# Performance work log

Measured on AMD Instinct MI355X. Metric: run time of the kernel, lower is better.

Reference implementation:

```python
import jax, jax.numpy as jnp
import numpy as np

ITERATIONS = 4

def setup_inputs() -> dict:
    key = jax.random.key(0)
    x = jax.random.normal(key, (16, 8192, 256), dtype=jnp.float32)
    return {"x": x}

def reference(x):
    # x: [B, S, D]; whiten features (last dim) using stats over axis=1 (sequence)
    B, S, D = x.shape
    m = jnp.mean(x, axis=1, keepdims=True)          # [B, 1, D]
    xn = x - m                                      # centered
    # covariance: [B, D, D]
    sigma = jnp.einsum('bsd,bse->bde', xn, xn) / (S - 1)
    # Newton-Schulz iteration for inverse matrix square root
    tr = jnp.trace(sigma, axis1=1, axis2=2)[:, None, None]   # [B,1,1]
    sigma_n = sigma / tr
    eye = jnp.eye(D, dtype=x.dtype)
    P = jnp.broadcast_to(eye, (B, D, D))
    for _ in range(ITERATIONS):
        P = 1.5 * P - 0.5 * (P @ P @ P @ sigma_n)
    wm = P / jnp.sqrt(tr)                           # whitening matrix [B, D, D]
    decorrelated = jnp.einsum('bsd,bde->bse', xn, wm)
    return decorrelated
```

## Files before the change

kernel.cpp:

```cpp
#include <hip/hip_runtime.h>

#define BB 16
#define SS 8192
#define DD 256

typedef __attribute__((ext_vector_type(8))) short bf16x8;
typedef __attribute__((ext_vector_type(4))) short bf16x4;
typedef __attribute__((ext_vector_type(4))) float f32x4;

__device__ __forceinline__ unsigned short f2bf(float f) {
    union { float f; unsigned u; } v; v.f = f;
    unsigned r = v.u + 0x7FFFu + ((v.u >> 16) & 1u);
    return (unsigned short)(r >> 16);
}
__device__ __forceinline__ float bf2f(unsigned short u) {
    union { unsigned u; float f; } cv; cv.u = (unsigned)u << 16; return cv.f;
}
__device__ __forceinline__ unsigned pack2(float a, float b) {
    return (unsigned)f2bf(a) | ((unsigned)f2bf(b) << 16);
}
__device__ __forceinline__ void split_bf(float w, unsigned short& hi, unsigned short& lo) {
    hi = f2bf(w);
    lo = f2bf(w - bf2f(hi));
}

#define LTS 40

__global__ __launch_bounds__(512) void moment_kernel(const float* __restrict__ x,
                                                     float* __restrict__ partial,
                                                     float* __restrict__ sumx8) {
    const int kc = blockIdx.x;
    const int nh = blockIdx.y;
    const int b  = blockIdx.z;
    const float* xb = x + ((size_t)b * SS + (size_t)kc * 1024) * DD;

    __shared__ unsigned short Lt0[256 * LTS];
    __shared__ unsigned short Lt1[256 * LTS];
    __shared__ float csh[8 * 256];

    const int tid  = threadIdx.x;
    const int wave = tid >> 6;
    const int lane = tid & 63;
    const int lc   = lane & 15;
    const int lq   = lane >> 4;

    const int mrow0 = (wave & 3) * 64;
    const int ncol0 = nh * 128 + (wave >> 2) * 64;

    const int sg = tid >> 6;
    const int dg = tid & 63;
    const float* xt = xb + (size_t)(sg * 4) * DD + dg;

    f32x4 acc[4][4];
#pragma unroll
    for (int mi = 0; mi < 4; ++mi)
#pragma unroll
        for (int ni = 0; ni < 4; ++ni) acc[mi][ni] = (f32x4){0.f, 0.f, 0.f, 0.f};
    float cs[4] = {0.f, 0.f, 0.f, 0.f};

    float va[16], vb[16];

    auto LOAD = [&](float* v, int t) {
#pragma unroll
        for (int i = 0; i < 4; ++i)
#pragma unroll
            for (int j = 0; j < 4; ++j)
                v[i * 4 + j] = xt[(size_t)(t * 32 + i) * DD + 64 * j];
    };
    auto STAGE = [&](const float* v, unsigned short* Lw) {
        if (nh == 0) {
#pragma unroll
            for (int j = 0; j < 4; ++j)
                cs[j] += v[j] + v[4 + j] + v[8 + j] + v[12 + j];
        }
#pragma unroll
        for (int j = 0; j < 4; ++j) {
            uint2 w;
            w.x = pack2(v[j], v[4 + j]);
            w.y = pack2(v[8 + j], v[12 + j]);
            *(uint2*)&Lw[(dg + 64 * j) * LTS + sg * 4] = w;
        }
    };
    auto COMPUTE = [&](const unsigned short* Lr) {
        bf16x8 af[4], bfr[4];
#pragma unroll
        for (int mi = 0; mi < 4; ++mi)
            af[mi] = *(const bf16x8*)&Lr[(mrow0 + mi * 16 + lc) * LTS + lq * 8];
#pragma unroll
        for (int ni = 0; ni < 4; ++ni)
            bfr[ni] = *(const bf16x8*)&Lr[(ncol0 + ni * 16 + lc) * LTS + lq * 8];
#pragma unroll
        for (int mi = 0; mi < 4; ++mi)
#pragma unroll
            for (int ni = 0; ni < 4; ++ni)
                acc[mi][ni] = __builtin_amdgcn_mfma_f32_16x16x32_bf16(
                    af[mi], bfr[ni], acc[mi][ni], 0, 0, 0);
    };

    LOAD(va, 0);
    STAGE(va, Lt0);
    LOAD(vb, 1);
    __syncthreads();

    for (int tt = 0; tt < 16; ++tt) {
        const int t0 = 2 * tt;
        STAGE(vb, Lt1);
        if (t0 < 30) LOAD(va, t0 + 2);
        COMPUTE(Lt0);
        __syncthreads();
        if (t0 + 1 < 31) STAGE(va, Lt0);
        if (t0 + 1 < 30) LOAD(vb, t0 + 3);
        COMPUTE(Lt1);
        __syncthreads();
    }

    float* pp = partial + (size_t)(kc * 16 + b) * DD * DD;
#pragma unroll
    for (int mi = 0; mi < 4; ++mi)
#pragma unroll
        for (int ni = 0; ni < 4; ++ni) {
            const int row = mrow0 + mi * 16 + lq * 4;
            const int col = ncol0 + ni * 16 + lc;
#pragma unroll
            for (int r = 0; r < 4; ++r)
                pp[(size_t)(row + r) * DD + col] = acc[mi][ni][r];
        }

    if (nh == 0) {
        __syncthreads();
#pragma unroll
        for (int j = 0; j < 4; ++j) csh[sg * 256 + dg + 64 * j] = cs[j];
        __syncthreads();
        if (tid < 256) {
            float t0 = 0.f;
#pragma unroll
            for (int g = 0; g < 8; ++g) t0 += csh[g * 256 + tid];
            sumx8[(size_t)(kc * 16 + b) * DD + tid] = t0;
        }
    }
}

__global__ __launch_bounds__(256) void stats_kernel(const float* __restrict__ partial,
                                                    const float* __restrict__ sumx8,
                                                    float* __restrict__ m,
                                                    float* __restrict__ trbuf) {
    const int b = blockIdx.x;
    const int d = threadIdx.x;
    float sx = 0.f;
#pragma unroll
    for (int kc = 0; kc < 8; ++kc)
        sx += sumx8[(size_t)(kc * 16 + b) * DD + d];
    const float mean = sx * (1.0f / (float)SS);
    m[b * DD + d] = mean;
    float ds = 0.f;
#pragma unroll
    for (int kc = 0; kc < 8; ++kc)
        ds += partial[((size_t)(kc * 16 + b) * DD + d) * DD + d];
    const float diag = (ds - (float)SS * mean * mean) * (1.0f / (float)(SS - 1));
    __shared__ float red[256];
    red[d] = diag;
    __syncthreads();
    for (int off = 128; off > 0; off >>= 1) {
        if (d < off) red[d] += red[d + off];
        __syncthreads();
    }
    if (d == 0) {
        const float tr = red[0];
        trbuf[b]      = tr;
        trbuf[16 + b] = rsqrtf(tr);
        trbuf[32 + b] = 1.0f / tr;
    }
}

__global__ __launch_bounds__(256) void sigman_kernel(const float* __restrict__ partial,
                                                     const float* __restrict__ m,
                                                     const float* __restrict__ trbuf,
                                                     float* __restrict__ Xa) {
    const int b = blockIdx.y;
    const int d = blockIdx.x;
    const int e = threadIdx.x;
    const float itr = trbuf[32 + b];
    const float md = m[b * DD + d];
    const float me = m[b * DD + e];
    float s = 0.f;
#pragma unroll
    for (int kc = 0; kc < 8; ++kc)
        s += partial[((size_t)(kc * 16 + b) * DD + d) * DD + e];
    Xa[(size_t)b * DD * DD + (size_t)d * DD + e] =
        (s - (float)SS * md * me) * (1.0f / (float)(SS - 1)) * itr;
}

#define BTS 72
__global__ __launch_bounds__(256) void bmm_mfma(
    const float* __restrict__ A0, const float* __restrict__ B0, float* __restrict__ C0,
    int ta0, int tb0,
    const float* __restrict__ A1, const float* __restrict__ B1, float* __restrict__ C1,
    int ta1, int tb1) {
    const int by  = blockIdx.y;
    const int set = by >> 4;
    const int bb  = by & 15;
    const float* Ag = (set ? A1 : A0) + (size_t)bb * DD * DD;
    const float* Bg = (set ? B1 : B0) + (size_t)bb * DD * DD;
    float*       Cg = (set ? C1 : C0) + (size_t)bb * DD * DD;
    const int TA = set ? ta1 : ta0;
    const int TB = set ? tb1 : tb0;

    const int m0 = (blockIdx.x >> 2) * 64;
    const int n0 = (blockIdx.x & 3) * 64;

    __shared__ unsigned short Ahi[2][64 * BTS];
    __shared__ unsigned short Alo[2][64 * BTS];
    __shared__ unsigned short Bhi[2][64 * BTS];
    __shared__ unsigned short Blo[2][64 * BTS];

    const int tid  = threadIdx.x;
    const int wave = tid >> 6;
    const int lane = tid & 63;
    const int lc = lane & 15, lq = lane >> 4;
    const int mrow0 = (wave & 1) * 32;
    const int ncol0 = (wave >> 1) * 32;

    const int r  = tid >> 2;
    const int kl = (tid & 3) * 4;
    const float* Arow = Ag + (size_t)(m0 + r) * DD + kl;
    const float* Brow = Bg + (size_t)(n0 + r) * DD + kl;

    f32x4 acc[2][2];
#pragma unroll
    for (int mi = 0; mi < 2; ++mi)
#pragma unroll
        for (int ni = 0; ni < 2; ++ni) acc[mi][ni] = (f32x4){0.f, 0.f, 0.f, 0.f};

    float4 va0[4], vb0[4], va1[4], vb1[4];

    auto LOADC = [&](float4* va, float4* vb, int c) {
#pragma unroll
        for (int i = 0; i < 4; ++i) va[i] = *(const float4*)(Arow + c * 64 + i * 16);
#pragma unroll
        for (int i = 0; i < 4; ++i) vb[i] = *(const float4*)(Brow + c * 64 + i * 16);
    };
    auto STAGE_SIDE = [&](const float4* v, unsigned short* Shi, unsigned short* Slo,
                          int c, int gmn, int tflag) {
#pragma unroll
        for (int i = 0; i < 4; ++i) {
            float xv[4] = {v[i].x, v[i].y, v[i].z, v[i].w};
            unsigned short h[4], l[4];
#pragma unroll
            for (int j = 0; j < 4; ++j) {
                float wv = xv[j];
                if (tflag) {
                    const int gk = c * 64 + kl + i * 16 + j;
                    wv = ((gk == gmn) ? 1.5f : 0.0f) - 0.5f * wv;
                }
                split_bf(wv, h[j], l[j]);
            }
            unsigned short* ph = &Shi[r * BTS + kl + i * 16];
            *(unsigned*)&ph[0] = (unsigned)h[0] | ((unsigned)h[1] << 16);
            *(unsigned*)&ph[2] = (unsigned)h[2] | ((unsigned)h[3] << 16);
            unsigned short* pl = &Slo[r * BTS + kl + i * 16];
            *(unsigned*)&pl[0] = (unsigned)l[0] | ((unsigned)l[1] << 16);
            *(unsigned*)&pl[2] = (unsigned)l[2] | ((unsigned)l[3] << 16);
        }
    };
    auto STAGE = [&](const float4* va, const float4* vb, int c, int buf) {
        STAGE_SIDE(va, Ahi[buf], Alo[buf], c, m0 + r, TA);
        STAGE_SIDE(vb, Bhi[buf], Blo[buf], c, n0 + r, TB);
    };
    auto COMPUTE = [&](int buf) {
#pragma unroll
        for (int ks = 0; ks < 2; ++ks) {
            bf16x8 ah[2], al[2], bh[2], bl[2];
#pragma unroll
            for (int mi = 0; mi < 2; ++mi) {
                const int off = (mrow0 + mi * 16 + lc) * BTS + ks * 32 + lq * 8;
                ah[mi] = *(const bf16x8*)&Ahi[buf][off];
                al[mi] = *(const bf16x8*)&Alo[buf][off];
            }
#pragma unroll
            for (int ni = 0; ni < 2; ++ni) {
                const int off = (ncol0 + ni * 16 + lc) * BTS + ks * 32 + lq * 8;
                bh[ni] = *(const bf16x8*)&Bhi[buf][off];
                bl[ni] = *(const bf16x8*)&Blo[buf][off];
            }
#pragma unroll
            for (int mi = 0; mi < 2; ++mi)
#pragma unroll
                for (int ni = 0; ni < 2; ++ni) {
                    acc[mi][ni] = __builtin_amdgcn_mfma_f32_16x16x32_bf16(
                        al[mi], bh[ni], acc[mi][ni], 0, 0, 0);
                    acc[mi][ni] = __builtin_amdgcn_mfma_f32_16x16x32_bf16(
                        ah[mi], bl[ni], acc[mi][ni], 0, 0, 0);
                    acc[mi][ni] = __builtin_amdgcn_mfma_f32_16x16x32_bf16(
                        ah[mi], bh[ni], acc[mi][ni], 0, 0, 0);
                }
        }
    };

    LOADC(va0, vb0, 0);
    LOADC(va1, vb1, 1);
    STAGE(va0, vb0, 0, 0);
    __syncthreads();
#pragma unroll
    for (int cc = 0; cc < 2; ++cc) {
        const int c0 = 2 * cc;
        STAGE(va1, vb1, c0 + 1, 1);
        if (c0 + 2 < 4) LOADC(va0, vb0, c0 + 2);
        COMPUTE(0);
        __syncthreads();
        if (c0 + 2 < 4) STAGE(va0, vb0, c0 + 2, 0);
        if (c0 + 3 < 4) LOADC(va1, vb1, c0 + 3);
        COMPUTE(1);
        __syncthreads();
    }

#pragma unroll
    for (int mi = 0; mi < 2; ++mi)
#pragma unroll
        for (int ni = 0; ni < 2; ++ni) {
            const int row = m0 + mrow0 + mi * 16 + lq * 4;
            const int col = n0 + ncol0 + ni * 16 + lc;
#pragma unroll
            for (int rr = 0; rr < 4; ++rr)
                Cg[(size_t)(row + rr) * DD + col] = acc[mi][ni][rr];
        }
}

#define BSS 264
__global__ __launch_bounds__(256) void apply_kernel(const float* __restrict__ x,
                                                    const float* __restrict__ P,
                                                    const float* __restrict__ m,
                                                    const float* __restrict__ trbuf,
                                                    float* __restrict__ out) {
    const int st = blockIdx.x;
    const int nh = blockIdx.y;
    const int b  = blockIdx.z;
    const int s0 = st * 128;
    const int n0 = nh * 128;
    const float rs = trbuf[16 + b];
    const float* xb = x + (size_t)b * SS * DD;
    const float* Pb = P + (size_t)b * DD * DD;
    const float* mb = m + b * DD;
    float* ob = out + (size_t)b * SS * DD;

    __shared__ unsigned short Bs[128 * BSS];
    __shared__ unsigned short As[128 * LTS];
    __shared__ float corr[128];

    const int tid  = threadIdx.x;
    const int wave = tid >> 6;
    const int lane = tid & 63;
    const int lc = lane & 15, lq = lane >> 4;
    const int mrow0 = (wave & 1) * 64;
    const int ncol0 = (wave >> 1) * 64;

    {
        const int r = tid >> 1, h = tid & 1;
        const float* prow = Pb + (size_t)(n0 + r) * DD + h * 128;
        unsigned short* brow = &Bs[r * BSS + h * 128];
#pragma unroll
        for (int i = 0; i < 32; ++i) {
            float4 pv = *(const float4*)(prow + i * 4);
            *(unsigned*)&brow[i * 4]     = pack2(pv.x * rs, pv.y * rs);
            *(unsigned*)&brow[i * 4 + 2] = pack2(pv.z * rs, pv.w * rs);
        }
    }
    __syncthreads();

    if (tid < 128) {
        float s = 0.f;
        for (int k = 0; k < 256; ++k)
            s += mb[k] * bf2f(Bs[tid * BSS + k]);
        corr[tid] = s;
    }

    f32x4 acc[4][4];
#pragma unroll
    for (int mi = 0; mi < 4; ++mi)
#pragma unroll
        for (int ni = 0; ni < 4; ++ni) acc[mi][ni] = (f32x4){0.f, 0.f, 0.f, 0.f};

    const int r8 = tid >> 3;
    const int d4 = (tid & 7) * 4;
    const float* xt = xb + (size_t)(s0 + r8) * DD + d4;

    float4 va[4], vb[4];

    auto LOAD = [&](float4* v, int t) {
#pragma unroll
        for (int i = 0; i < 4; ++i)
            v[i] = *(const float4*)(xt + (size_t)t * 32 + (size_t)i * 32 * DD);
    };
    auto STAGE = [&](const float4* v) {
#pragma unroll
        for (int i = 0; i < 4; ++i) {
            uint2 w;
            w.x = pack2(v[i].x, v[i].y);
            w.y = pack2(v[i].z, v[i].w);
            *(uint2*)&As[(r8 + i * 32) * LTS + d4] = w;
        }
    };
    auto COMPUTE = [&](int t) {
        const int k0 = t * 32;
        bf16x8 af[4], bfr[4];
#pragma unroll
        for (int mi = 0; mi < 4; ++mi)
            af[mi] = *(const bf16x8*)&As[(mrow0 + mi * 16 + lc) * LTS + lq * 8];
#pragma unroll
        for (int ni = 0; ni < 4; ++ni)
            bfr[ni] = *(const bf16x8*)&Bs[(ncol0 + ni * 16 + lc) * BSS + k0 + lq * 8];
#pragma unroll
        for (int mi = 0; mi < 4; ++mi)
#pragma unroll
            for (int ni = 0; ni < 4; ++ni)
                acc[mi][ni] = __builtin_amdgcn_mfma_f32_16x16x32_bf16(
                    af[mi], bfr[ni], acc[mi][ni], 0, 0, 0);
    };

    LOAD(va, 0);
#pragma unroll
    for (int tt = 0; tt < 4; ++tt) {
        const int t0 = 2 * tt;
        __syncthreads();
        STAGE(va);
        if (t0 + 1 < 8) LOAD(vb, t0 + 1);
        __syncthreads();
        COMPUTE(t0);
        __syncthreads();
        STAGE(vb);
        if (t0 + 2 < 8) LOAD(va, t0 + 2);
        __syncthreads();
        COMPUTE(t0 + 1);
    }

#pragma unroll
    for (int mi = 0; mi < 4; ++mi)
#pragma unroll
        for (int ni = 0; ni < 4; ++ni) {
            const int row = s0 + mrow0 + mi * 16 + lq * 4;
            const int col = n0 + ncol0 + ni * 16 + lc;
            const float cv = corr[ncol0 + ni * 16 + lc];
#pragma unroll
            for (int r = 0; r < 4; ++r)
                ob[(size_t)(row + r) * DD + col] = acc[mi][ni][r] - cv;
        }
}

extern "C" void kernel_launch(void* const* d_in, const int* in_sizes, int n_in,
                              void* d_out, int out_size, void* d_ws, size_t ws_size,
                              hipStream_t stream) {
    const float* x = (const float*)d_in[0];
    float* out = (float*)d_out;
    float* ws = (float*)d_ws;

    const size_t MAT = (size_t)BB * DD * DD;
    float* partial = ws;
    float* sumx8 = partial + 8 * MAT;
    float* m     = sumx8 + 8 * BB * DD;
    float* trbuf = m + BB * DD;
    float* Xa    = trbuf + 64;
    float* Xb    = Xa + MAT;
    float* T     = Xb + MAT;
    float* Pa    = T + MAT;
    float* Pb    = Pa + MAT;

    moment_kernel<<<dim3(8, 2, 16), 512, 0, stream>>>(x, partial, sumx8);
    stats_kernel<<<16, 256, 0, stream>>>(partial, sumx8, m, trbuf);
    sigman_kernel<<<dim3(256, 16), 256, 0, stream>>>(partial, m, trbuf, Xa);

    bmm_mfma<<<dim3(16, 16), 256, 0, stream>>>(Xa, Xa, T, 1, 1,
                                               Xa, Xa, T, 1, 1);
    bmm_mfma<<<dim3(16, 16), 256, 0, stream>>>(Xa, T, Xb, 0, 0,
                                               Xa, T, Xb, 0, 0);
    bmm_mfma<<<dim3(16, 32), 256, 0, stream>>>(Xa, Xb, Pa, 1, 1,
                                               Xb, Xb, T, 1, 1);
    bmm_mfma<<<dim3(16, 16), 256, 0, stream>>>(Xb, T, Xa, 0, 0,
                                               Xb, T, Xa, 0, 0);
    bmm_mfma<<<dim3(16, 32), 256, 0, stream>>>(Pa, Xa, Pb, 0, 1,
                                               Xa, Xa, T, 1, 1);
    bmm_mfma<<<dim3(16, 16), 256, 0, stream>>>(Xa, T, Xb, 0, 0,
                                               Xa, T, Xb, 0, 0);
    bmm_mfma<<<dim3(16, 16), 256, 0, stream>>>(Pb, Xb, Pa, 0, 1,
                                               Pb, Xb, Pa, 0, 1);

    apply_kernel<<<dim3(64, 2, 16), 256, 0, stream>>>(x, Pa, m, trbuf, out);
}
```

Measured before the change: 379.1 us.

## Fuse stats into sigman kernel and load apply A-fragments directly from global

Merges the trace/mean stats kernel and the normalized-covariance kernel into one finalize kernel, where each block recomputes the mean and trace redundantly and then writes 16 rows of sigma_n. This removes one launch and the serial dependency between them. The apply kernel now loads x straight into MFMA A-fragment registers in bf16 and drops the LDS staging and the four barriers per iteration pair. The mean-correction dot product is also split across all 256 threads. The risks are less coalesced global reads of x in the apply kernel and redundant trace reductions in every finalize block.

After: 412.9 us. 1.09x slower.

```diff
diff --git a/kernel.cpp b/kernel.cpp
--- a/kernel.cpp
+++ b/kernel.cpp
@@ -1,4 +1,5 @@
 #include <hip/hip_runtime.h>
+#include <hip/hip_bf16.h>
 
 #define BB 16
 #define SS 8192
@@ -140,54 +141,57 @@
     }
 }
 
-__global__ __launch_bounds__(256) void stats_kernel(const float* __restrict__ partial,
-                                                    const float* __restrict__ sumx8,
-                                                    float* __restrict__ m,
-                                                    float* __restrict__ trbuf) {
-    const int b = blockIdx.x;
-    const int d = threadIdx.x;
+__global__ __launch_bounds__(256) void finalize_kernel(const float* __restrict__ partial,
+                                                       const float* __restrict__ sumx8,
+                                                       float* __restrict__ m,
+                                                       float* __restrict__ trbuf,
+                                                       float* __restrict__ Xa) {
+    const int g = blockIdx.x;
+    const int b = blockIdx.y;
+    const int t = threadIdx.x;
+
+    __shared__ float mean[256];
+    __shared__ float red[256];
+
     float sx = 0.f;
 #pragma unroll
     for (int kc = 0; kc < 8; ++kc)
-        sx += sumx8[(size_t)(kc * 16 + b) * DD + d];
-    const float mean = sx * (1.0f / (float)SS);
-    m[b * DD + d] = mean;
+        sx += sumx8[(size_t)(kc * 16 + b) * DD + t];
+    const float mu = sx * (1.0f / (float)SS);
+    mean[t] = mu;
+    if (g == 0) m[b * DD + t] = mu;
+
     float ds = 0.f;
 #pragma unroll
     for (int kc = 0; kc < 8; ++kc)
-        ds += partial[((size_t)(kc * 16 + b) * DD + d) * DD + d];
-    const float diag = (ds - (float)SS * mean * mean) * (1.0f / (float)(SS - 1));
-    __shared__ float red[256];
-    red[d] = diag;
+        ds += partial[((size_t)(kc * 16 + b) * DD + t) * DD + t];
+    red[t] = (ds - (float)SS * mu * mu) * (1.0f / (float)(SS - 1));
     __syncthreads();
     for (int off = 128; off > 0; off >>= 1) {
-        if (d < off) red[d] += red[d + off];
-        __syncthreads();
-    }
-    if (d == 0) {
-        const float tr = red[0];
+        if (t < off) red[t] += red[t + off];
+        __syncthreads();
+    }
+    const float tr  = red[0];
+    const float itr = 1.0f / tr;
+    if (g == 0 && t == 0) {
         trbuf[b]      = tr;
         trbuf[16 + b] = rsqrtf(tr);
-        trbuf[32 + b] = 1.0f / tr;
-    }
-}
-
-__global__ __launch_bounds__(256) void sigman_kernel(const float* __restrict__ partial,
-                                                     const float* __restrict__ m,
-                                                     const float* __restrict__ trbuf,
-                                                     float* __restrict__ Xa) {
-    const int b = blockIdx.y;
-    const int d = blockIdx.x;
-    const int e = threadIdx.x;
-    const float itr = trbuf[32 + b];
-    const float md = m[b * DD + d];
-    const float me = m[b * DD + e];
-    float s = 0.f;
-#pragma unroll
-    for (int kc = 0; kc < 8; ++kc)
-        s += partial[((size_t)(kc * 16 + b) * DD + d) * DD + e];
-    Xa[(size_t)b * DD * DD + (size_t)d * DD + e] =
-        (s - (float)SS * md * me) * (1.0f / (float)(SS - 1)) * itr;
+        trbuf[32 + b] = itr;
+    }
+
+    const float sc = (1.0f / (float)(SS - 1)) * itr;
+    const float mt = mean[t];
+#pragma unroll
+    for (int i = 0; i < 16; ++i) {
+        const int d = g * 16 + i;
+        const float md = mean[d];
+        float s = 0.f;
+#pragma unroll
+        for (int kc = 0; kc < 8; ++kc)
+            s += partial[((size_t)(kc * 16 + b) * DD + d) * DD + t];
+        Xa[(size_t)b * DD * DD + (size_t)d * DD + t] =
+            (s - (float)SS * md * mt) * sc;
+    }
 }
 
 #define BTS 72
@@ -343,7 +347,7 @@
     float* ob = out + (size_t)b * SS * DD;
 
     __shared__ unsigned short Bs[128 * BSS];
-    __shared__ unsigned short As[128 * LTS];
+    __shared__ float corr2[256];
     __shared__ float corr[128];
 
     const int tid  = threadIdx.x;
@@ -366,12 +370,16 @@
     }
     __syncthreads();
 
-    if (tid < 128) {
+    {
+        const int n = tid & 127, h = tid >> 7;
         float s = 0.f;
-        for (int k = 0; k < 256; ++k)
-            s += mb[k] * bf2f(Bs[tid * BSS + k]);
-        corr[tid] = s;
-    }
+#pragma unroll 8
+        for (int k = 0; k < 128; ++k)
+            s += mb[h * 128 + k] * bf2f(Bs[n * BSS + h * 128 + k]);
+        corr2[tid] = s;
+    }
+    __syncthreads();
+    if (tid < 128) corr[tid] = corr2[tid] + corr2[128 + tid];
 
     f32x4 acc[4][4];
 #pragma unroll
@@ -379,35 +387,31 @@
 #pragma unroll
         for (int ni = 0; ni < 4; ++ni) acc[mi][ni] = (f32x4){0.f, 0.f, 0.f, 0.f};
 
-    const int r8 = tid >> 3;
-    const int d4 = (tid & 7) * 4;
-    const float* xt = xb + (size_t)(s0 + r8) * DD + d4;
-
-    float4 va[4], vb[4];
-
-    auto LOAD = [&](float4* v, int t) {
-#pragma unroll
-        for (int i = 0; i < 4; ++i)
-            v[i] = *(const float4*)(xt + (size_t)t * 32 + (size_t)i * 32 * DD);
-    };
-    auto STAGE = [&](const float4* v) {
-#pragma unroll
-        for (int i = 0; i < 4; ++i) {
-            uint2 w;
-            w.x = pack2(v[i].x, v[i].y);
-            w.y = pack2(v[i].z, v[i].w);
-            *(uint2*)&As[(r8 + i * 32) * LTS + d4] = w;
-        }
-    };
-    auto COMPUTE = [&](int t) {
-        const int k0 = t * 32;
+    const float* xw = xb + (size_t)(s0 + mrow0 + lc) * DD + lq * 8;
+    float4 cA[8], nA[8];
+
+    auto LOADA = [&](float4* v, int t) {
+#pragma unroll
+        for (int mi = 0; mi < 4; ++mi) {
+            const float* p = xw + (size_t)mi * 16 * DD + t * 32;
+            v[mi * 2]     = *(const float4*)p;
+            v[mi * 2 + 1] = *(const float4*)(p + 4);
+        }
+    };
+    auto STEP = [&](const float4* v, int t) {
         bf16x8 af[4], bfr[4];
 #pragma unroll
-        for (int mi = 0; mi < 4; ++mi)
-            af[mi] = *(const bf16x8*)&As[(mrow0 + mi * 16 + lc) * LTS + lq * 8];
+        for (int mi = 0; mi < 4; ++mi) {
+            union { bf16x8 w; __hip_bfloat162 h2[4]; } u;
+            u.h2[0] = __float22bfloat162_rn(make_float2(v[mi * 2].x,     v[mi * 2].y));
+            u.h2[1] = __float22bfloat162_rn(make_float2(v[mi * 2].z,     v[mi * 2].w));
+            u.h2[2] = __float22bfloat162_rn(make_float2(v[mi * 2 + 1].x, v[mi * 2 + 1].y));
+            u.h2[3] = __float22bfloat162_rn(make_float2(v[mi * 2 + 1].z, v[mi * 2 + 1].w));
+            af[mi] = u.w;
+        }
 #pragma unroll
         for (int ni = 0; ni < 4; ++ni)
-            bfr[ni] = *(const bf16x8*)&Bs[(ncol0 + ni * 16 + lc) * BSS + k0 + lq * 8];
+            bfr[ni] = *(const bf16x8*)&Bs[(ncol0 + ni * 16 + lc) * BSS + t * 32 + lq * 8];
 #pragma unroll
         for (int mi = 0; mi < 4; ++mi)
 #pragma unroll
@@ -416,22 +420,17 @@
                     af[mi], bfr[ni], acc[mi][ni], 0, 0, 0);
     };
 
-    LOAD(va, 0);
+    LOADA(cA, 0);
 #pragma unroll
     for (int tt = 0; tt < 4; ++tt) {
         const int t0 = 2 * tt;
-        __syncthreads();
-        STAGE(va);
-        if (t0 + 1 < 8) LOAD(vb, t0 + 1);
-        __syncthreads();
-        COMPUTE(t0);
-        __syncthreads();
-        STAGE(vb);
-        if (t0 + 2 < 8) LOAD(va, t0 + 2);
-        __syncthreads();
-        COMPUTE(t0 + 1);
-    }
-
+        if (t0 + 1 < 8) LOADA(nA, t0 + 1);
+        STEP(cA, t0);
+        if (t0 + 2 < 8) LOADA(cA, t0 + 2);
+        STEP(nA, t0 + 1);
+    }
+
+    __syncthreads();
 #pragma unroll
     for (int mi = 0; mi < 4; ++mi)
 #pragma unroll
@@ -464,8 +463,7 @@
     float* Pb    = Pa + MAT;
 
     moment_kernel<<<dim3(8, 2, 16), 512, 0, stream>>>(x, partial, sumx8);
-    stats_kernel<<<16, 256, 0, stream>>>(partial, sumx8, m, trbuf);
-    sigman_kernel<<<dim3(256, 16), 256, 0, stream>>>(partial, m, trbuf, Xa);
+    finalize_kernel<<<dim3(16, 16), 256, 0, stream>>>(partial, sumx8, m, trbuf, Xa);
 
     bmm_mfma<<<dim3(16, 16), 256, 0, stream>>>(Xa, Xa, T, 1, 1,
                                                Xa, Xa, T, 1, 1);
```
